# Kernel optimization log

Hardware: AMD Instinct MI355X
Metric: run time of the kernel (lower is better)

Reference implementation:

```python
import jax, jax.numpy as jnp
import numpy as np

B, N, K = 32, 511, 2          # trees per batch, nodes per tree (full binary), max children
IN_DIM, MEM_DIM = 256, 256


def _build_children_idx():
    # Heap tree (node p has children 2p+1, 2p+2), relabeled i -> N-1-i so that every
    # child id < parent id; then a single pass i = 0..N-1 is a valid topological order
    # (leaves first, root last at index N-1). Padded child slots are -1.
    ch = np.full((N, K), -1, dtype=np.int64)
    for p in range(N):
        for k in range(K):
            c = 2 * p + 1 + k
            if c < N:
                ch[N - 1 - p, k] = N - 1 - c
    return jnp.asarray(ch)


def setup_inputs() -> dict:
    key = jax.random.key(0)
    ks = jax.random.split(key, 9)
    s_in = float(1.0 / np.sqrt(IN_DIM))   # torch Linear default init bound
    s_m = float(1.0 / np.sqrt(MEM_DIM))
    u = lambda k, shape, s: jax.random.uniform(k, shape, jnp.float32, -s, s)
    return {
        "inputs": jax.random.normal(ks[0], (B, N, IN_DIM), jnp.float32),
        "W_ioux": u(ks[1], (3 * MEM_DIM, IN_DIM), s_in),
        "b_ioux": u(ks[2], (3 * MEM_DIM,), s_in),
        "W_iouh": u(ks[3], (3 * MEM_DIM, MEM_DIM), s_m),
        "b_iouh": u(ks[4], (3 * MEM_DIM,), s_m),
        "W_fx": u(ks[5], (MEM_DIM, IN_DIM), s_in),
        "b_fx": u(ks[6], (MEM_DIM,), s_in),
        "W_fh": u(ks[7], (MEM_DIM, MEM_DIM), s_m),
        "b_fh": u(ks[8], (MEM_DIM,), s_m),
        "children_idx": _build_children_idx(),
    }


def reference(inputs, W_ioux, b_ioux, W_iouh, b_iouh, W_fx, b_fx, W_fh, b_fh,
              children_idx):
    # Input-only projections depend on no recurrent state -> one big GEMM up front.
    x_iou = jnp.einsum('bni,oi->nbo', inputs, W_ioux) + b_ioux   # [N,B,3M]
    x_f = jnp.einsum('bni,mi->nbm', inputs, W_fx) + b_fx          # [N,B,M]

    def step(carry, xs):
        c_buf, h_buf, idx = carry                  # [N,B,M], [N,B,M], scalar node id
        ch, xi, xf = xs                            # [K], [B,3M], [B,M]
        valid = ch >= 0
        mask = valid.astype(c_buf.dtype)[:, None, None]
        safe = jnp.where(valid, ch, 0)
        child_c = c_buf[safe] * mask               # [K,B,M] (zeros for padded / leaf)
        child_h = h_buf[safe] * mask               # [K,B,M]
        h_sum = child_h.sum(0)                     # [B,M]  (child-sum)
        iou = xi + h_sum @ W_iouh.T + b_iouh       # [B,3M]
        i, o, u = jnp.split(iou, 3, axis=-1)
        i, o, u = jax.nn.sigmoid(i), jax.nn.sigmoid(o), jnp.tanh(u)
        # per-child forget gate: fh(child_h) + fx(inputs) broadcast over children
        f = jax.nn.sigmoid(jnp.einsum('kbm,nm->kbn', child_h, W_fh) + b_fh + xf[None])
        c = i * u + (f * child_c).sum(0)           # [B,M]
        h = o * jnp.tanh(c)
        c_buf = c_buf.at[idx].set(c)
        h_buf = h_buf.at[idx].set(h)
        return (c_buf, h_buf, idx + 1), None

    zeros = jnp.zeros((N, B, MEM_DIM), inputs.dtype)
    (c_buf, h_buf, _), _ = jax.lax.scan(
        step, (zeros, zeros, jnp.int32(0)), (children_idx, x_iou, x_f))

    root_c = c_buf[N - 1]                # [B,M]
    root_h = h_buf[N - 1]                # [B,M]
    hiddens = h_buf.transpose(1, 0, 2)   # [B,N,M]: h of node i at row i (tree.idx == i)
    return root_c, root_h, hiddens
```

## Files before the change

kernel.cpp:

```cpp
#include <hip/hip_runtime.h>
#include <hip/hip_bf16.h>


#define NN 511
#define BB 32
#define DD 256

typedef __attribute__((ext_vector_type(8))) short short8;
typedef __attribute__((ext_vector_type(4))) short short4v;
typedef __attribute__((ext_vector_type(4))) float f32x4;

#define MFMA __builtin_amdgcn_mfma_f32_16x16x32_bf16

#define OFF_XBF   0UL
#define OFF_HBF   8372224UL
#define OFF_CBUF  16744448UL
#define OFF_WCAT  33488896UL
#define OFF_BIAS  34537472UL

__device__ __forceinline__ short f2bf(float f) {
    union { float f; unsigned int u; } v; v.f = f;
    unsigned int r = (v.u + 0x7FFFu + ((v.u >> 16) & 1u)) >> 16;
    return (short)(unsigned short)r;
}
__device__ __forceinline__ float sigmf(float x) { return 1.0f / (1.0f + __expf(-x)); }
__device__ __forceinline__ float tanhc(float x) {
    x = fminf(fmaxf(x, -15.f), 15.f);
    float e = __expf(2.f * x);
    return (e - 1.f) / (e + 1.f);
}

__global__ void prep_all(const float* __restrict__ inp,
                         const float* __restrict__ Wix, const float* __restrict__ Wih,
                         const float* __restrict__ Wfx, const float* __restrict__ Wfh,
                         const float* __restrict__ bix, const float* __restrict__ bih,
                         const float* __restrict__ bfx, const float* __restrict__ bfh,
                         short* __restrict__ xbf, short* __restrict__ wcat,
                         float* __restrict__ bias) {
    const int tid = threadIdx.x;
    for (int v = blockIdx.x; v < 4088 + 2048; v += gridDim.x) {
        if (v < 4088) {
            int idx = v * 256 + tid;
            int n = idx / (BB * 64);
            int rem = idx - n * (BB * 64);
            int b = rem >> 6;
            int c4 = rem & 63;
            float4 w = ((const float4*)(inp + ((long)b * NN + n) * DD))[c4];
            short4v sv = { f2bf(w.x), f2bf(w.y), f2bf(w.z), f2bf(w.w) };
            *(short4v*)(xbf + (long)idx * 4) = sv;
        } else {
            int t = (v - 4088) * 256 + tid;
            int row = t >> 9, c = t & 511;
            float w;
            if (c < 256) w = (row < 768) ? Wix[row * 256 + c] : Wfx[(row - 768) * 256 + c];
            else         w = (row < 768) ? Wih[row * 256 + (c - 256)]
                                         : Wfh[(row - 768) * 256 + (c - 256)];
            wcat[t] = f2bf(w);
            if (c == 0)
                bias[row] = (row < 768) ? (bix[row] + bih[row])
                                        : (bfx[row - 768] + bfh[row - 768]);
        }
    }
}


__global__ __launch_bounds__(256, 4) void xproj(
    const short* __restrict__ xbf, const short* __restrict__ wcat,
    const float* __restrict__ bias, short* __restrict__ hbf,
    float* __restrict__ cbuf, float* __restrict__ out) {
    __shared__ short lb[3 * 16 * 256];
    const int tid = threadIdx.x;
    const int mt = blockIdx.y;
    for (int u = tid; u < 3 * 16 * 32; u += 256) {
        const int s = u >> 9;
        const int rr = (u >> 5) & 15;
        const int k = (u & 31) * 8;
        short8 v = *(const short8*)(wcat + ((long)(s * 256 + mt * 16 + rr) * 512 + k));
        *(short8*)(lb + (s * 16 + rr) * 256 + (k ^ ((rr & 7) << 3))) = v;
    }
    __syncthreads();

    const int lane = tid & 63;
    const int wid = tid >> 6;
    const int rt = blockIdx.x * 4 + wid;
    if (rt >= 512) return;
    const int arow = lane & 15;
    const int kgrp = lane >> 4;
    const int node = rt >> 1;
    const int bh = rt & 1;
    const int m = mt * 16 + arow;
    const int swz = (arow & 7) << 3;

    const short* ap = xbf + ((long)rt * 16 + arow) * DD + kgrp * 8;
    short8 a[8];
#pragma unroll
    for (int ks = 0; ks < 8; ++ks) a[ks] = *(const short8*)(ap + ks * 32);

    f32x4 ai = {0.f, 0.f, 0.f, 0.f}, ao = ai, au = ai;
    const short* b0 = lb + (0 * 16 + arow) * 256;
    const short* b1 = lb + (1 * 16 + arow) * 256;
    const short* b2 = lb + (2 * 16 + arow) * 256;
#pragma unroll
    for (int ks = 0; ks < 8; ++ks) {
        const int ko = (ks * 32 + kgrp * 8) ^ swz;
        ai = MFMA(a[ks], *(const short8*)(b0 + ko), ai, 0, 0, 0);
        ao = MFMA(a[ks], *(const short8*)(b1 + ko), ao, 0, 0, 0);
        au = MFMA(a[ks], *(const short8*)(b2 + ko), au, 0, 0, 0);
    }

    const float bi = bias[m], bo = bias[256 + m], bu = bias[512 + m];
#pragma unroll
    for (int r = 0; r < 4; ++r) {
        const int b = bh * 16 + kgrp * 4 + r;
        const float iv = sigmf(ai[r] + bi);
        const float ov = sigmf(ao[r] + bo);
        const float uv = tanhc(au[r] + bu);
        const float c = iv * uv;
        const float h = ov * tanhc(c);
        const long rowg = (long)node * BB + b;
        cbuf[rowg * DD + m] = c;
        hbf[rowg * DD + m] = f2bf(h);
        out[2 * BB * DD + ((long)b * NN + node) * DD + m] = h;
    }
}

__global__ __launch_bounds__(256, 2) void level_h(
    const short* __restrict__ xbf, const short* __restrict__ wcat,
    const float* __restrict__ bias, short* __restrict__ hbf,
    float* __restrict__ cbuf, float* __restrict__ out, int istart, int ntasks) {
    __shared__ short lb[4 * 16 * 512];
    const int tid = threadIdx.x;
    const int mt = blockIdx.y;
#pragma unroll
    for (int it = 0; it < 16; ++it) {
        const int u = it * 256 + tid;
        const int s = u >> 10;
        const int r = (u >> 6) & 15;
        const int k = (u & 63) * 8;
        short8 v = *(const short8*)(wcat + ((long)(s * 256 + mt * 16 + r) * 512 + k));
        *(short8*)(lb + (s * 16 + r) * 512 + (k ^ ((r & 7) << 3))) = v;
    }
    __syncthreads();

    const int lane = tid & 63;
    const int wid = tid >> 6;
    const int rt = blockIdx.x * 4 + wid;
    if (rt >= ntasks) return;
    const int arow = lane & 15;
    const int kgrp = lane >> 4;
    const int node = istart + (rt >> 1);
    const int bh = rt & 1;
    const int m = mt * 16 + arow;
    const int swz = (arow & 7) << 3;
    const int c0 = 2 * node - 511, c1 = 2 * node - 512;
    const short* b0 = lb + (0 * 16 + arow) * 512;
    const short* b1 = lb + (1 * 16 + arow) * 512;
    const short* b2 = lb + (2 * 16 + arow) * 512;
    const short* b3 = lb + (3 * 16 + arow) * 512;

    f32x4 ai = {0.f, 0.f, 0.f, 0.f}, ao = ai, au = ai, afx = ai, af0 = ai, af1 = ai;

    {
        const short* ap = xbf + ((long)(node * BB + bh * 16) + arow) * DD + kgrp * 8;
        short8 a[8];
#pragma unroll
        for (int ks = 0; ks < 8; ++ks) a[ks] = *(const short8*)(ap + ks * 32);
#pragma unroll
        for (int ks = 0; ks < 8; ++ks) {
            const int ko = (ks * 32 + kgrp * 8) ^ swz;
            ai = MFMA(a[ks], *(const short8*)(b0 + ko), ai, 0, 0, 0);
            ao = MFMA(a[ks], *(const short8*)(b1 + ko), ao, 0, 0, 0);
            au = MFMA(a[ks], *(const short8*)(b2 + ko), au, 0, 0, 0);
            afx = MFMA(a[ks], *(const short8*)(b3 + ko), afx, 0, 0, 0);
        }
    }
    {
        const short* ap0 = hbf + ((long)(c0 * BB + bh * 16) + arow) * DD + kgrp * 8;
        const short* ap1 = hbf + ((long)(c1 * BB + bh * 16) + arow) * DD + kgrp * 8;
        short8 a0[8], a1[8];
#pragma unroll
        for (int ks = 0; ks < 8; ++ks) {
            a0[ks] = *(const short8*)(ap0 + ks * 32);
            a1[ks] = *(const short8*)(ap1 + ks * 32);
        }
#pragma unroll
        for (int ks = 0; ks < 8; ++ks) {
            const int ko = 256 + ((ks * 32 + kgrp * 8) ^ swz);
            short8 wi = *(const short8*)(b0 + ko);
            short8 wo = *(const short8*)(b1 + ko);
            short8 wu = *(const short8*)(b2 + ko);
            short8 wf = *(const short8*)(b3 + ko);
            ai = MFMA(a0[ks], wi, ai, 0, 0, 0);
            ai = MFMA(a1[ks], wi, ai, 0, 0, 0);
            ao = MFMA(a0[ks], wo, ao, 0, 0, 0);
            ao = MFMA(a1[ks], wo, ao, 0, 0, 0);
            au = MFMA(a0[ks], wu, au, 0, 0, 0);
            au = MFMA(a1[ks], wu, au, 0, 0, 0);
            af0 = MFMA(a0[ks], wf, af0, 0, 0, 0);
            af1 = MFMA(a1[ks], wf, af1, 0, 0, 0);
        }
    }

    const float bi = bias[m], bo = bias[256 + m], bu = bias[512 + m], bf = bias[768 + m];
#pragma unroll
    for (int r = 0; r < 4; ++r) {
        const int b = bh * 16 + kgrp * 4 + r;
        const float iv = sigmf(ai[r] + bi);
        const float ov = sigmf(ao[r] + bo);
        const float uv = tanhc(au[r] + bu);
        const float f0 = sigmf(afx[r] + af0[r] + bf);
        const float f1 = sigmf(afx[r] + af1[r] + bf);
        const float cc0 = cbuf[((long)c0 * BB + b) * DD + m];
        const float cc1 = cbuf[((long)c1 * BB + b) * DD + m];
        const float c = iv * uv + f0 * cc0 + f1 * cc1;
        const float h = ov * tanhc(c);
        const long rowg = (long)node * BB + b;
        cbuf[rowg * DD + m] = c;
        hbf[rowg * DD + m] = f2bf(h);
        out[2 * BB * DD + ((long)b * NN + node) * DD + m] = h;
        if (node == NN - 1) {
            out[b * DD + m] = c;
            out[BB * DD + b * DD + m] = h;
        }
    }
}

extern "C" void kernel_launch(void* const* d_in, const int* in_sizes, int n_in,
                              void* d_out, int out_size, void* d_ws, size_t ws_size,
                              hipStream_t stream) {
    (void)in_sizes; (void)n_in; (void)out_size; (void)ws_size;
    const float* inputs = (const float*)d_in[0];
    const float* W_ioux = (const float*)d_in[1];
    const float* b_ioux = (const float*)d_in[2];
    const float* W_iouh = (const float*)d_in[3];
    const float* b_iouh = (const float*)d_in[4];
    const float* W_fx = (const float*)d_in[5];
    const float* b_fx = (const float*)d_in[6];
    const float* W_fh = (const float*)d_in[7];
    const float* b_fh = (const float*)d_in[8];

    char* ws = (char*)d_ws;
    short* xbf = (short*)(ws + OFF_XBF);
    short* hbf = (short*)(ws + OFF_HBF);
    float* cbuf = (float*)(ws + OFF_CBUF);
    short* wcat = (short*)(ws + OFF_WCAT);
    float* bias = (float*)(ws + OFF_BIAS);
    float* outp = (float*)d_out;

    prep_all<<<dim3(2048), dim3(256), 0, stream>>>(
        inputs, W_ioux, W_iouh, W_fx, W_fh, b_ioux, b_iouh, b_fx, b_fh,
        xbf, wcat, bias);

    xproj<<<dim3(128, 16), dim3(256), 0, stream>>>(xbf, wcat, bias, hbf, cbuf, outp);

    for (int d = 7; d >= 0; --d) {
        const int istart = 512 - (1 << (d + 1));
        const int ntasks = (1 << d) * 2;
        level_h<<<dim3((ntasks + 3) / 4, 16), dim3(256), 0, stream>>>(
            xbf, wcat, bias, hbf, cbuf, outp, istart, ntasks);
    }
}
```

Baseline: 100.3 us.

## Load weight tiles via global_load_lds and use grid-stride loops with capped grids

```diff
diff --git a/kernel.cpp b/kernel.cpp
--- a/kernel.cpp
+++ b/kernel.cpp
@@ -11,6 +11,9 @@
 typedef __attribute__((ext_vector_type(4))) float f32x4;
 
 #define MFMA __builtin_amdgcn_mfma_f32_16x16x32_bf16
+
+typedef __attribute__((address_space(3))) void lds_void_t;
+typedef const __attribute__((address_space(1))) void glob_void_t;
 
 #define OFF_XBF   0UL
 #define OFF_HBF   8372224UL
@@ -67,60 +70,67 @@
 __global__ __launch_bounds__(256, 4) void xproj(
     const short* __restrict__ xbf, const short* __restrict__ wcat,
     const float* __restrict__ bias, short* __restrict__ hbf,
-    float* __restrict__ cbuf, float* __restrict__ out) {
+    float* __restrict__ cbuf, float* __restrict__ out, int ntasks) {
     __shared__ short lb[3 * 16 * 256];
     const int tid = threadIdx.x;
     const int mt = blockIdx.y;
-    for (int u = tid; u < 3 * 16 * 32; u += 256) {
+#pragma unroll
+    for (int it = 0; it < 6; ++it) {
+        const int u = it * 256 + tid;
         const int s = u >> 9;
         const int rr = (u >> 5) & 15;
         const int k = (u & 31) * 8;
-        short8 v = *(const short8*)(wcat + ((long)(s * 256 + mt * 16 + rr) * 512 + k));
-        *(short8*)(lb + (s * 16 + rr) * 256 + (k ^ ((rr & 7) << 3))) = v;
+        const short* src = wcat + ((long)(s * 256 + mt * 16 + rr) * 512
+                                   + (k ^ ((rr & 7) << 3)));
+        __builtin_amdgcn_global_load_lds((glob_void_t*)src,
+            (lds_void_t*)(lb + (it * 256 + (tid >> 6) * 64) * 8), 16, 0, 0);
     }
     __syncthreads();
 
     const int lane = tid & 63;
     const int wid = tid >> 6;
-    const int rt = blockIdx.x * 4 + wid;
-    if (rt >= 512) return;
+    const int slot = blockIdx.x * 4 + wid;
+    const int nslots = gridDim.x * 4;
     const int arow = lane & 15;
     const int kgrp = lane >> 4;
-    const int node = rt >> 1;
-    const int bh = rt & 1;
     const int m = mt * 16 + arow;
     const int swz = (arow & 7) << 3;
-
-    const short* ap = xbf + ((long)rt * 16 + arow) * DD + kgrp * 8;
-    short8 a[8];
-#pragma unroll
-    for (int ks = 0; ks < 8; ++ks) a[ks] = *(const short8*)(ap + ks * 32);
-
-    f32x4 ai = {0.f, 0.f, 0.f, 0.f}, ao = ai, au = ai;
     const short* b0 = lb + (0 * 16 + arow) * 256;
     const short* b1 = lb + (1 * 16 + arow) * 256;
     const short* b2 = lb + (2 * 16 + arow) * 256;
-#pragma unroll
-    for (int ks = 0; ks < 8; ++ks) {
-        const int ko = (ks * 32 + kgrp * 8) ^ swz;
-        ai = MFMA(a[ks], *(const short8*)(b0 + ko), ai, 0, 0, 0);
-        ao = MFMA(a[ks], *(const short8*)(b1 + ko), ao, 0, 0, 0);
-        au = MFMA(a[ks], *(const short8*)(b2 + ko), au, 0, 0, 0);
-    }
-
     const float bi = bias[m], bo = bias[256 + m], bu = bias[512 + m];
-#pragma unroll
-    for (int r = 0; r < 4; ++r) {
-        const int b = bh * 16 + kgrp * 4 + r;
-        const float iv = sigmf(ai[r] + bi);
-        const float ov = sigmf(ao[r] + bo);
-        const float uv = tanhc(au[r] + bu);
-        const float c = iv * uv;
-        const float h = ov * tanhc(c);
-        const long rowg = (long)node * BB + b;
-        cbuf[rowg * DD + m] = c;
-        hbf[rowg * DD + m] = f2bf(h);
-        out[2 * BB * DD + ((long)b * NN + node) * DD + m] = h;
+
+    for (int rt = slot; rt < ntasks; rt += nslots) {
+        const int node = rt >> 1;
+        const int bh = rt & 1;
+
+        const short* ap = xbf + ((long)rt * 16 + arow) * DD + kgrp * 8;
+        short8 a[8];
+#pragma unroll
+        for (int ks = 0; ks < 8; ++ks) a[ks] = *(const short8*)(ap + ks * 32);
+
+        f32x4 ai = {0.f, 0.f, 0.f, 0.f}, ao = ai, au = ai;
+#pragma unroll
+        for (int ks = 0; ks < 8; ++ks) {
+            const int ko = (ks * 32 + kgrp * 8) ^ swz;
+            ai = MFMA(a[ks], *(const short8*)(b0 + ko), ai, 0, 0, 0);
+            ao = MFMA(a[ks], *(const short8*)(b1 + ko), ao, 0, 0, 0);
+            au = MFMA(a[ks], *(const short8*)(b2 + ko), au, 0, 0, 0);
+        }
+
+#pragma unroll
+        for (int r = 0; r < 4; ++r) {
+            const int b = bh * 16 + kgrp * 4 + r;
+            const float iv = sigmf(ai[r] + bi);
+            const float ov = sigmf(ao[r] + bo);
+            const float uv = tanhc(au[r] + bu);
+            const float c = iv * uv;
+            const float h = ov * tanhc(c);
+            const long rowg = (long)node * BB + b;
+            cbuf[rowg * DD + m] = c;
+            hbf[rowg * DD + m] = f2bf(h);
+            out[2 * BB * DD + ((long)b * NN + node) * DD + m] = h;
+        }
     }
 }
 
@@ -135,92 +145,97 @@
     for (int it = 0; it < 16; ++it) {
         const int u = it * 256 + tid;
         const int s = u >> 10;
-        const int r = (u >> 6) & 15;
+        const int rr = (u >> 6) & 15;
         const int k = (u & 63) * 8;
-        short8 v = *(const short8*)(wcat + ((long)(s * 256 + mt * 16 + r) * 512 + k));
-        *(short8*)(lb + (s * 16 + r) * 512 + (k ^ ((r & 7) << 3))) = v;
+        const short* src = wcat + ((long)(s * 256 + mt * 16 + rr) * 512
+                                   + (k ^ ((rr & 7) << 3)));
+        __builtin_amdgcn_global_load_lds((glob_void_t*)src,
+            (lds_void_t*)(lb + (it * 256 + (tid >> 6) * 64) * 8), 16, 0, 0);
     }
     __syncthreads();
 
     const int lane = tid & 63;
     const int wid = tid >> 6;
-    const int rt = blockIdx.x * 4 + wid;
-    if (rt >= ntasks) return;
+    const int slot = blockIdx.x * 4 + wid;
+    const int nslots = gridDim.x * 4;
     const int arow = lane & 15;
     const int kgrp = lane >> 4;
-    const int node = istart + (rt >> 1);
-    const int bh = rt & 1;
     const int m = mt * 16 + arow;
     const int swz = (arow & 7) << 3;
-    const int c0 = 2 * node - 511, c1 = 2 * node - 512;
     const short* b0 = lb + (0 * 16 + arow) * 512;
     const short* b1 = lb + (1 * 16 + arow) * 512;
     const short* b2 = lb + (2 * 16 + arow) * 512;
     const short* b3 = lb + (3 * 16 + arow) * 512;
-
-    f32x4 ai = {0.f, 0.f, 0.f, 0.f}, ao = ai, au = ai, afx = ai, af0 = ai, af1 = ai;
-
-    {
-        const short* ap = xbf + ((long)(node * BB + bh * 16) + arow) * DD + kgrp * 8;
-        short8 a[8];
-#pragma unroll
-        for (int ks = 0; ks < 8; ++ks) a[ks] = *(const short8*)(ap + ks * 32);
-#pragma unroll
-        for (int ks = 0; ks < 8; ++ks) {
-            const int ko = (ks * 32 + kgrp * 8) ^ swz;
-            ai = MFMA(a[ks], *(const short8*)(b0 + ko), ai, 0, 0, 0);
-            ao = MFMA(a[ks], *(const short8*)(b1 + ko), ao, 0, 0, 0);
-            au = MFMA(a[ks], *(const short8*)(b2 + ko), au, 0, 0, 0);
-            afx = MFMA(a[ks], *(const short8*)(b3 + ko), afx, 0, 0, 0);
-        }
-    }
-    {
-        const short* ap0 = hbf + ((long)(c0 * BB + bh * 16) + arow) * DD + kgrp * 8;
-        const short* ap1 = hbf + ((long)(c1 * BB + bh * 16) + arow) * DD + kgrp * 8;
-        short8 a0[8], a1[8];
-#pragma unroll
-        for (int ks = 0; ks < 8; ++ks) {
-            a0[ks] = *(const short8*)(ap0 + ks * 32);
-            a1[ks] = *(const short8*)(ap1 + ks * 32);
-        }
-#pragma unroll
-        for (int ks = 0; ks < 8; ++ks) {
-            const int ko = 256 + ((ks * 32 + kgrp * 8) ^ swz);
-            short8 wi = *(const short8*)(b0 + ko);
-            short8 wo = *(const short8*)(b1 + ko);
-            short8 wu = *(const short8*)(b2 + ko);
-            short8 wf = *(const short8*)(b3 + ko);
-            ai = MFMA(a0[ks], wi, ai, 0, 0, 0);
-            ai = MFMA(a1[ks], wi, ai, 0, 0, 0);
-            ao = MFMA(a0[ks], wo, ao, 0, 0, 0);
-            ao = MFMA(a1[ks], wo, ao, 0, 0, 0);
-            au = MFMA(a0[ks], wu, au, 0, 0, 0);
-            au = MFMA(a1[ks], wu, au, 0, 0, 0);
-            af0 = MFMA(a0[ks], wf, af0, 0, 0, 0);
-            af1 = MFMA(a1[ks], wf, af1, 0, 0, 0);
-        }
-    }
-
     const float bi = bias[m], bo = bias[256 + m], bu = bias[512 + m], bf = bias[768 + m];
-#pragma unroll
-    for (int r = 0; r < 4; ++r) {
-        const int b = bh * 16 + kgrp * 4 + r;
-        const float iv = sigmf(ai[r] + bi);
-        const float ov = sigmf(ao[r] + bo);
-        const float uv = tanhc(au[r] + bu);
-        const float f0 = sigmf(afx[r] + af0[r] + bf);
-        const float f1 = sigmf(afx[r] + af1[r] + bf);
-        const float cc0 = cbuf[((long)c0 * BB + b) * DD + m];
-        const float cc1 = cbuf[((long)c1 * BB + b) * DD + m];
-        const float c = iv * uv + f0 * cc0 + f1 * cc1;
-        const float h = ov * tanhc(c);
-        const long rowg = (long)node * BB + b;
-        cbuf[rowg * DD + m] = c;
-        hbf[rowg * DD + m] = f2bf(h);
-        out[2 * BB * DD + ((long)b * NN + node) * DD + m] = h;
-        if (node == NN - 1) {
-            out[b * DD + m] = c;
-            out[BB * DD + b * DD + m] = h;
+
+    for (int rt = slot; rt < ntasks; rt += nslots) {
+        const int node = istart + (rt >> 1);
+        const int bh = rt & 1;
+        const int c0 = 2 * node - 511, c1 = 2 * node - 512;
+
+        f32x4 ai = {0.f, 0.f, 0.f, 0.f}, ao = ai, au = ai, afx = ai, af0 = ai, af1 = ai;
+
+        {
+            const short* ap = xbf + ((long)(node * BB + bh * 16) + arow) * DD + kgrp * 8;
+            short8 a[8];
+#pragma unroll
+            for (int ks = 0; ks < 8; ++ks) a[ks] = *(const short8*)(ap + ks * 32);
+#pragma unroll
+            for (int ks = 0; ks < 8; ++ks) {
+                const int ko = (ks * 32 + kgrp * 8) ^ swz;
+                ai = MFMA(a[ks], *(const short8*)(b0 + ko), ai, 0, 0, 0);
+                ao = MFMA(a[ks], *(const short8*)(b1 + ko), ao, 0, 0, 0);
+                au = MFMA(a[ks], *(const short8*)(b2 + ko), au, 0, 0, 0);
+                afx = MFMA(a[ks], *(const short8*)(b3 + ko), afx, 0, 0, 0);
+            }
+        }
+        {
+            const short* ap0 = hbf + ((long)(c0 * BB + bh * 16) + arow) * DD + kgrp * 8;
+            const short* ap1 = hbf + ((long)(c1 * BB + bh * 16) + arow) * DD + kgrp * 8;
+            short8 a0[8], a1[8];
+#pragma unroll
+            for (int ks = 0; ks < 8; ++ks) {
+                a0[ks] = *(const short8*)(ap0 + ks * 32);
+                a1[ks] = *(const short8*)(ap1 + ks * 32);
+            }
+#pragma unroll
+            for (int ks = 0; ks < 8; ++ks) {
+                const int ko = 256 + ((ks * 32 + kgrp * 8) ^ swz);
+                short8 wi = *(const short8*)(b0 + ko);
+                short8 wo = *(const short8*)(b1 + ko);
+                short8 wu = *(const short8*)(b2 + ko);
+                short8 wf = *(const short8*)(b3 + ko);
+                ai = MFMA(a0[ks], wi, ai, 0, 0, 0);
+                ai = MFMA(a1[ks], wi, ai, 0, 0, 0);
+                ao = MFMA(a0[ks], wo, ao, 0, 0, 0);
+                ao = MFMA(a1[ks], wo, ao, 0, 0, 0);
+                au = MFMA(a0[ks], wu, au, 0, 0, 0);
+                au = MFMA(a1[ks], wu, au, 0, 0, 0);
+                af0 = MFMA(a0[ks], wf, af0, 0, 0, 0);
+                af1 = MFMA(a1[ks], wf, af1, 0, 0, 0);
+            }
+        }
+
+#pragma unroll
+        for (int r = 0; r < 4; ++r) {
+            const int b = bh * 16 + kgrp * 4 + r;
+            const float iv = sigmf(ai[r] + bi);
+            const float ov = sigmf(ao[r] + bo);
+            const float uv = tanhc(au[r] + bu);
+            const float f0 = sigmf(afx[r] + af0[r] + bf);
+            const float f1 = sigmf(afx[r] + af1[r] + bf);
+            const float cc0 = cbuf[((long)c0 * BB + b) * DD + m];
+            const float cc1 = cbuf[((long)c1 * BB + b) * DD + m];
+            const float c = iv * uv + f0 * cc0 + f1 * cc1;
+            const float h = ov * tanhc(c);
+            const long rowg = (long)node * BB + b;
+            cbuf[rowg * DD + m] = c;
+            hbf[rowg * DD + m] = f2bf(h);
+            out[2 * BB * DD + ((long)b * NN + node) * DD + m] = h;
+            if (node == NN - 1) {
+                out[b * DD + m] = c;
+                out[BB * DD + b * DD + m] = h;
+            }
         }
     }
 }
@@ -251,12 +266,14 @@
         inputs, W_ioux, W_iouh, W_fx, W_fh, b_ioux, b_iouh, b_fx, b_fh,
         xbf, wcat, bias);
 
-    xproj<<<dim3(128, 16), dim3(256), 0, stream>>>(xbf, wcat, bias, hbf, cbuf, outp);
+    xproj<<<dim3(64, 16), dim3(256), 0, stream>>>(
+        xbf, wcat, bias, hbf, cbuf, outp, 512);
 
     for (int d = 7; d >= 0; --d) {
         const int istart = 512 - (1 << (d + 1));
         const int ntasks = (1 << d) * 2;
-        level_h<<<dim3((ntasks + 3) / 4, 16), dim3(256), 0, stream>>>(
+        int gx = (ntasks + 3) / 4; if (gx > 32) gx = 32;
+        level_h<<<dim3(gx, 16), dim3(256), 0, stream>>>(
             xbf, wcat, bias, hbf, cbuf, outp, istart, ntasks);
     }
 }
```

New measurement: 180.7 us. +80.1%, slower.

## Process both batch halves per wave to reuse LDS weight fragments

Applied to the files above, without the earlier changes.

```diff
diff --git a/kernel.cpp b/kernel.cpp
--- a/kernel.cpp
+++ b/kernel.cpp
@@ -127,7 +127,7 @@
 __global__ __launch_bounds__(256, 2) void level_h(
     const short* __restrict__ xbf, const short* __restrict__ wcat,
     const float* __restrict__ bias, short* __restrict__ hbf,
-    float* __restrict__ cbuf, float* __restrict__ out, int istart, int ntasks) {
+    float* __restrict__ cbuf, float* __restrict__ out, int istart, int ncount) {
     __shared__ short lb[4 * 16 * 512];
     const int tid = threadIdx.x;
     const int mt = blockIdx.y;
@@ -135,21 +135,20 @@
     for (int it = 0; it < 16; ++it) {
         const int u = it * 256 + tid;
         const int s = u >> 10;
-        const int r = (u >> 6) & 15;
+        const int rr = (u >> 6) & 15;
         const int k = (u & 63) * 8;
-        short8 v = *(const short8*)(wcat + ((long)(s * 256 + mt * 16 + r) * 512 + k));
-        *(short8*)(lb + (s * 16 + r) * 512 + (k ^ ((r & 7) << 3))) = v;
+        short8 v = *(const short8*)(wcat + ((long)(s * 256 + mt * 16 + rr) * 512 + k));
+        *(short8*)(lb + (s * 16 + rr) * 512 + (k ^ ((rr & 7) << 3))) = v;
     }
     __syncthreads();
 
     const int lane = tid & 63;
     const int wid = tid >> 6;
-    const int rt = blockIdx.x * 4 + wid;
-    if (rt >= ntasks) return;
+    const int p = blockIdx.x * 4 + wid;
+    if (p >= ncount) return;
     const int arow = lane & 15;
     const int kgrp = lane >> 4;
-    const int node = istart + (rt >> 1);
-    const int bh = rt & 1;
+    const int node = istart + p;
     const int m = mt * 16 + arow;
     const int swz = (arow & 7) << 3;
     const int c0 = 2 * node - 511, c1 = 2 * node - 512;
@@ -158,71 +157,96 @@
     const short* b2 = lb + (2 * 16 + arow) * 512;
     const short* b3 = lb + (3 * 16 + arow) * 512;
 
-    f32x4 ai = {0.f, 0.f, 0.f, 0.f}, ao = ai, au = ai, afx = ai, af0 = ai, af1 = ai;
-
-    {
-        const short* ap = xbf + ((long)(node * BB + bh * 16) + arow) * DD + kgrp * 8;
-        short8 a[8];
-#pragma unroll
-        for (int ks = 0; ks < 8; ++ks) a[ks] = *(const short8*)(ap + ks * 32);
-#pragma unroll
-        for (int ks = 0; ks < 8; ++ks) {
-            const int ko = (ks * 32 + kgrp * 8) ^ swz;
-            ai = MFMA(a[ks], *(const short8*)(b0 + ko), ai, 0, 0, 0);
-            ao = MFMA(a[ks], *(const short8*)(b1 + ko), ao, 0, 0, 0);
-            au = MFMA(a[ks], *(const short8*)(b2 + ko), au, 0, 0, 0);
-            afx = MFMA(a[ks], *(const short8*)(b3 + ko), afx, 0, 0, 0);
-        }
-    }
-    {
-        const short* ap0 = hbf + ((long)(c0 * BB + bh * 16) + arow) * DD + kgrp * 8;
-        const short* ap1 = hbf + ((long)(c1 * BB + bh * 16) + arow) * DD + kgrp * 8;
-        short8 a0[8], a1[8];
-#pragma unroll
-        for (int ks = 0; ks < 8; ++ks) {
-            a0[ks] = *(const short8*)(ap0 + ks * 32);
-            a1[ks] = *(const short8*)(ap1 + ks * 32);
-        }
-#pragma unroll
-        for (int ks = 0; ks < 8; ++ks) {
-            const int ko = 256 + ((ks * 32 + kgrp * 8) ^ swz);
+    const f32x4 z = {0.f, 0.f, 0.f, 0.f};
+    f32x4 ai[2] = {z, z}, ao[2] = {z, z}, au[2] = {z, z};
+    f32x4 af0[2] = {z, z}, af1[2];
+
+    const short* axb = xbf + (long)node * BB * DD + (long)arow * DD + kgrp * 8;
+#pragma unroll
+    for (int ch = 0; ch < 2; ++ch) {
+        short8 a[2][4];
+#pragma unroll
+        for (int ks = 0; ks < 4; ++ks)
+#pragma unroll
+            for (int h2 = 0; h2 < 2; ++h2)
+                a[h2][ks] = *(const short8*)(axb + h2 * 16 * DD + (ch * 4 + ks) * 32);
+#pragma unroll
+        for (int ks = 0; ks < 4; ++ks) {
+            const int ko = ((ch * 4 + ks) * 32 + kgrp * 8) ^ swz;
             short8 wi = *(const short8*)(b0 + ko);
             short8 wo = *(const short8*)(b1 + ko);
             short8 wu = *(const short8*)(b2 + ko);
             short8 wf = *(const short8*)(b3 + ko);
-            ai = MFMA(a0[ks], wi, ai, 0, 0, 0);
-            ai = MFMA(a1[ks], wi, ai, 0, 0, 0);
-            ao = MFMA(a0[ks], wo, ao, 0, 0, 0);
-            ao = MFMA(a1[ks], wo, ao, 0, 0, 0);
-            au = MFMA(a0[ks], wu, au, 0, 0, 0);
-            au = MFMA(a1[ks], wu, au, 0, 0, 0);
-            af0 = MFMA(a0[ks], wf, af0, 0, 0, 0);
-            af1 = MFMA(a1[ks], wf, af1, 0, 0, 0);
+#pragma unroll
+            for (int h2 = 0; h2 < 2; ++h2) {
+                ai[h2] = MFMA(a[h2][ks], wi, ai[h2], 0, 0, 0);
+                ao[h2] = MFMA(a[h2][ks], wo, ao[h2], 0, 0, 0);
+                au[h2] = MFMA(a[h2][ks], wu, au[h2], 0, 0, 0);
+                af0[h2] = MFMA(a[h2][ks], wf, af0[h2], 0, 0, 0);
+            }
+        }
+    }
+    af1[0] = af0[0];
+    af1[1] = af0[1];
+
+    const short* h0b = hbf + (long)c0 * BB * DD + (long)arow * DD + kgrp * 8;
+    const short* h1b = hbf + (long)c1 * BB * DD + (long)arow * DD + kgrp * 8;
+#pragma unroll
+    for (int ch = 0; ch < 4; ++ch) {
+        short8 a0[2][2], a1[2][2];
+#pragma unroll
+        for (int ks = 0; ks < 2; ++ks)
+#pragma unroll
+            for (int h2 = 0; h2 < 2; ++h2) {
+                const long off = h2 * 16 * DD + (ch * 2 + ks) * 32;
+                a0[h2][ks] = *(const short8*)(h0b + off);
+                a1[h2][ks] = *(const short8*)(h1b + off);
+            }
+#pragma unroll
+        for (int ks = 0; ks < 2; ++ks) {
+            const int ko = 256 + (((ch * 2 + ks) * 32 + kgrp * 8) ^ swz);
+            short8 wi = *(const short8*)(b0 + ko);
+            short8 wo = *(const short8*)(b1 + ko);
+            short8 wu = *(const short8*)(b2 + ko);
+            short8 wf = *(const short8*)(b3 + ko);
+#pragma unroll
+            for (int h2 = 0; h2 < 2; ++h2) {
+                ai[h2] = MFMA(a0[h2][ks], wi, ai[h2], 0, 0, 0);
+                ai[h2] = MFMA(a1[h2][ks], wi, ai[h2], 0, 0, 0);
+                ao[h2] = MFMA(a0[h2][ks], wo, ao[h2], 0, 0, 0);
+                ao[h2] = MFMA(a1[h2][ks], wo, ao[h2], 0, 0, 0);
+                au[h2] = MFMA(a0[h2][ks], wu, au[h2], 0, 0, 0);
+                au[h2] = MFMA(a1[h2][ks], wu, au[h2], 0, 0, 0);
+                af0[h2] = MFMA(a0[h2][ks], wf, af0[h2], 0, 0, 0);
+                af1[h2] = MFMA(a1[h2][ks], wf, af1[h2], 0, 0, 0);
+            }
         }
     }
 
     const float bi = bias[m], bo = bias[256 + m], bu = bias[512 + m], bf = bias[768 + m];
 #pragma unroll
-    for (int r = 0; r < 4; ++r) {
-        const int b = bh * 16 + kgrp * 4 + r;
-        const float iv = sigmf(ai[r] + bi);
-        const float ov = sigmf(ao[r] + bo);
-        const float uv = tanhc(au[r] + bu);
-        const float f0 = sigmf(afx[r] + af0[r] + bf);
-        const float f1 = sigmf(afx[r] + af1[r] + bf);
-        const float cc0 = cbuf[((long)c0 * BB + b) * DD + m];
-        const float cc1 = cbuf[((long)c1 * BB + b) * DD + m];
-        const float c = iv * uv + f0 * cc0 + f1 * cc1;
-        const float h = ov * tanhc(c);
-        const long rowg = (long)node * BB + b;
-        cbuf[rowg * DD + m] = c;
-        hbf[rowg * DD + m] = f2bf(h);
-        out[2 * BB * DD + ((long)b * NN + node) * DD + m] = h;
-        if (node == NN - 1) {
-            out[b * DD + m] = c;
-            out[BB * DD + b * DD + m] = h;
-        }
-    }
+    for (int h2 = 0; h2 < 2; ++h2)
+#pragma unroll
+        for (int r = 0; r < 4; ++r) {
+            const int b = h2 * 16 + kgrp * 4 + r;
+            const float iv = sigmf(ai[h2][r] + bi);
+            const float ov = sigmf(ao[h2][r] + bo);
+            const float uv = tanhc(au[h2][r] + bu);
+            const float f0 = sigmf(af0[h2][r] + bf);
+            const float f1 = sigmf(af1[h2][r] + bf);
+            const float cc0 = cbuf[((long)c0 * BB + b) * DD + m];
+            const float cc1 = cbuf[((long)c1 * BB + b) * DD + m];
+            const float c = iv * uv + f0 * cc0 + f1 * cc1;
+            const float h = ov * tanhc(c);
+            const long rowg = (long)node * BB + b;
+            cbuf[rowg * DD + m] = c;
+            hbf[rowg * DD + m] = f2bf(h);
+            out[2 * BB * DD + ((long)b * NN + node) * DD + m] = h;
+            if (node == NN - 1) {
+                out[b * DD + m] = c;
+                out[BB * DD + b * DD + m] = h;
+            }
+        }
 }
 
 extern "C" void kernel_launch(void* const* d_in, const int* in_sizes, int n_in,
@@ -255,8 +279,8 @@
 
     for (int d = 7; d >= 0; --d) {
         const int istart = 512 - (1 << (d + 1));
-        const int ntasks = (1 << d) * 2;
-        level_h<<<dim3((ntasks + 3) / 4, 16), dim3(256), 0, stream>>>(
-            xbf, wcat, bias, hbf, cbuf, outp, istart, ntasks);
-    }
-}
+        const int ncount = 1 << d;
+        level_h<<<dim3((ncount + 3) / 4, 16), dim3(256), 0, stream>>>(
+            xbf, wcat, bias, hbf, cbuf, outp, istart, ncount);
+    }
+}
```

After: 123.8 us. +23.4%, slower.
